# Kernel optimization log

Measured on AMD Instinct MI355X. Metric: run time of the kernel, lower is better.

Reference implementation:

```python
import jax, jax.numpy as jnp
import numpy as np
import math

IN_F = 2048
INTER_F = 8192
OUT_F = 2048
STRIPE = 256
N_STRIPES = INTER_F // STRIPE
EPS = 1e-7
BETA = 0.99
STEPS = 1000.0
THRESH_LR_SCALE = 1.0 * math.sqrt(IN_F)


def setup_inputs() -> dict:
    key = jax.random.key(0)
    ks = jax.random.split(key, 8)
    x = jax.random.normal(ks[0], (2, 1024, IN_F), dtype=jnp.float32)
    gate_weight = jax.random.normal(ks[1], (IN_F, INTER_F), dtype=jnp.float32) / math.sqrt(IN_F)
    gate_bias = jnp.zeros((INTER_F,), dtype=jnp.float32)
    # thresholds ~ threshold_init scale so the mask is non-trivially sparse
    gate_thresholds = jax.random.uniform(ks[2], (N_STRIPES, IN_F), dtype=jnp.float32) * (0.1 / THRESH_LR_SCALE) * 20.0
    med = jax.random.normal(ks[3], (IN_F,), dtype=jnp.float32) * 0.01
    aad = jax.random.uniform(ks[4], (IN_F,), dtype=jnp.float32) + 0.5
    up_weight = jax.random.normal(ks[5], (IN_F, INTER_F), dtype=jnp.float32) * 0.02
    up_bias = jnp.zeros((INTER_F,), dtype=jnp.float32)
    down_weight = jax.random.normal(ks[6], (OUT_F, INTER_F), dtype=jnp.float32) / math.sqrt(INTER_F)
    down_bias = jnp.zeros((OUT_F,), dtype=jnp.float32)
    return dict(x=x, gate_weight=gate_weight, gate_bias=gate_bias,
                gate_thresholds=gate_thresholds, med=med, aad=aad,
                up_weight=up_weight, up_bias=up_bias,
                down_weight=down_weight, down_bias=down_bias)


def _cwic_linear(xf, weight, bias, thresholds, med, aad):
    # eval-mode CWICLinear. xf: [T, I]
    debiaser = 1.0 / (EPS + (1.0 - BETA ** STEPS))
    mu = med * debiaser                                   # [I]
    std = aad * debiaser / math.sqrt(2.0 * math.pi)      # [I]
    thr = thresholds * std[None, :] * THRESH_LR_SCALE     # [N, I]
    xd = xf - mu[None, :]                                 # [T, I]
    mask = (jnp.abs(xd)[:, None, :] > thr[None]).astype(xf.dtype)  # [T, N, I]
    xm = xd[:, None, :] * mask + mu[None, None, :]        # [T, N, I]
    w = weight.T.reshape(N_STRIPES, STRIPE, IN_F)          # [N, S, I]
    y = jnp.einsum('nsi,tni->tns', w, xm).reshape(-1, INTER_F) + bias[None, :]
    active = STRIPE * mask.reshape(xf.shape[0], -1).sum(axis=-1)  # [T]
    dense = jnp.full_like(active, STRIPE * N_STRIPES * IN_F)
    return y, dense, active


def reference(x, gate_weight, gate_bias, gate_thresholds, med, aad,
              up_weight, up_bias, down_weight, down_bias):
    B, T, I = x.shape
    xf = x.reshape(-1, I)
    g, dense, active = _cwic_linear(xf, gate_weight, gate_bias, gate_thresholds, med, aad)
    up = xf @ up_weight + up_bias[None, :]                 # Conv1D: x @ W + b
    h = jax.nn.silu(g) * up                                # [BT, inter]
    y = h @ down_weight.T + down_bias[None, :]             # nn.Linear
    return (y.reshape(B, T, OUT_F), dense.reshape(B, T), active.reshape(B, T))
```

## Files before the change

kernel.cpp:

```cpp
#include <hip/hip_runtime.h>
#include <math.h>
#include <stdint.h>

typedef __bf16 bf16_t;
typedef __bf16 bf16x8 __attribute__((ext_vector_type(8)));
typedef __bf16 bf16x4 __attribute__((ext_vector_type(4)));
typedef float f32x4 __attribute__((ext_vector_type(4)));
typedef short s16x8 __attribute__((ext_vector_type(8)));

#define TOKS 2048
#define INF 2048
#define JNF 8192
#define ONF 2048

#define VMW(N) asm volatile("s_waitcnt vmcnt(" #N ")" ::: "memory")
#define LGKM0 asm volatile("s_waitcnt lgkmcnt(0)" ::: "memory")
#define BAR __builtin_amdgcn_s_barrier()


__device__ __forceinline__ void gld(const bf16_t* g, bf16_t* l) {
  __builtin_amdgcn_global_load_lds((const __attribute__((address_space(1))) void*)g,
                                   (__attribute__((address_space(3))) void*)l, 16, 0, 0);
}
__device__ __forceinline__ void stage2(const bf16_t* p0, const bf16_t* p1, bf16_t* l) {
  gld(p0, l);
  gld(p1, l + 4096);
}

template <int Q>
__device__ __forceinline__ void ds_afq(const bf16_t* A, int a0, int a1, bf16x8 (&af)[2][2]) {
  af[0][0] = *(const bf16x8*)&A[a0 + (Q * 32) * 64];
  af[0][1] = *(const bf16x8*)&A[a1 + (Q * 32) * 64];
  af[1][0] = *(const bf16x8*)&A[a0 + (Q * 32 + 16) * 64];
  af[1][1] = *(const bf16x8*)&A[a1 + (Q * 32 + 16) * 64];
}

__device__ __forceinline__ void ds_bfq(const bf16_t* B, int b0, int b1, bf16x8 (&bfr)[4][2]) {
#pragma unroll
  for (int ni = 0; ni < 4; ++ni) {
    bfr[ni][0] = *(const bf16x8*)&B[b0 + ni * 16 * 64];
    bfr[ni][1] = *(const bf16x8*)&B[b1 + ni * 16 * 64];
  }
}

template <int P>
__device__ __forceinline__ void mfma_ph(f32x4 (&acc)[8][4], const bf16x8 (&af)[2][2],
                                        const bf16x8 (&bfr)[4][2]) {
  constexpr int Q = P & 3;
  __builtin_amdgcn_s_barrier();
  __builtin_amdgcn_s_setprio(1);
#pragma unroll
  for (int mi2 = 0; mi2 < 2; ++mi2)
#pragma unroll
    for (int ni = 0; ni < 4; ++ni)
#pragma unroll
      for (int ks = 0; ks < 2; ++ks)
        acc[Q * 2 + mi2][ni] = __builtin_amdgcn_mfma_f32_16x16x32_bf16(
            af[mi2][ks], bfr[ni][ks], acc[Q * 2 + mi2][ni], 0, 0, 0);
  __builtin_amdgcn_s_setprio(0);
}

__device__ __forceinline__ void mask_tile(bf16_t* At, const bf16_t* Thl,
                                          int ktile, int me0, int kq8) {
  const s16x8 ABS = {0x7FFF, 0x7FFF, 0x7FFF, 0x7FFF, 0x7FFF, 0x7FFF, 0x7FFF, 0x7FFF};
  s16x8 t = *(const s16x8*)&Thl[ktile + kq8];
#pragma unroll
  for (int h = 0; h < 2; ++h)
#pragma unroll
    for (int r = 0; r < 2; ++r) {
      int off = me0 + h * 8192 + r * 4096;
      s16x8 a = *(const s16x8*)&At[off];
      s16x8 m = (s16x8)((t - (a & ABS)) >> 15);
      *(s16x8*)&At[off] = a & m;
    }
}


__global__ __launch_bounds__(256) void prep_mu_thr(
    const float* __restrict__ med, const float* __restrict__ aad,
    const float* __restrict__ gth, float debiaser,
    float* __restrict__ mu, float* __restrict__ thr, bf16_t* __restrict__ thrb) {
  int gid = blockIdx.x * 256 + threadIdx.x;
  if (gid < INF) mu[gid] = med[gid] * debiaser;
  int i = gid & (INF - 1);
  float stdv = aad[i] * debiaser / 2.5066282746310002f;
  float tv = gth[gid] * stdv * 45.254833995939045f;
  thr[gid] = tv;
  thrb[gid] = (bf16_t)tv;
}

__global__ __launch_bounds__(256) void prep_x_count(
    const float* __restrict__ x, const float* __restrict__ mu,
    const float* __restrict__ thr,
    bf16_t* __restrict__ xb, bf16_t* __restrict__ xdb,
    float* __restrict__ dense, float* __restrict__ active) {
  int t = blockIdx.x;
  int tid = threadIdx.x;
  int i0 = tid * 8;
  const float* xrow = x + (size_t)t * INF;
  f32x4 x0 = *(const f32x4*)&xrow[i0];
  f32x4 x1 = *(const f32x4*)&xrow[i0 + 4];
  f32x4 m0 = *(const f32x4*)&mu[i0];
  f32x4 m1 = *(const f32x4*)&mu[i0 + 4];
  f32x4 d0 = x0 - m0, d1 = x1 - m1;
  bf16x8 ox, od;
  ox[0] = (bf16_t)x0[0]; ox[1] = (bf16_t)x0[1]; ox[2] = (bf16_t)x0[2]; ox[3] = (bf16_t)x0[3];
  ox[4] = (bf16_t)x1[0]; ox[5] = (bf16_t)x1[1]; ox[6] = (bf16_t)x1[2]; ox[7] = (bf16_t)x1[3];
  od[0] = (bf16_t)d0[0]; od[1] = (bf16_t)d0[1]; od[2] = (bf16_t)d0[2]; od[3] = (bf16_t)d0[3];
  od[4] = (bf16_t)d1[0]; od[5] = (bf16_t)d1[1]; od[6] = (bf16_t)d1[2]; od[7] = (bf16_t)d1[3];
  *(bf16x8*)&xb[(size_t)t * INF + i0] = ox;
  *(bf16x8*)&xdb[(size_t)t * INF + i0] = od;
  f32x4 a0, a1;
  a0[0] = fabsf(d0[0]); a0[1] = fabsf(d0[1]); a0[2] = fabsf(d0[2]); a0[3] = fabsf(d0[3]);
  a1[0] = fabsf(d1[0]); a1[1] = fabsf(d1[1]); a1[2] = fabsf(d1[2]); a1[3] = fabsf(d1[3]);
  int cnt = 0;
#pragma unroll 4
  for (int n = 0; n < 32; ++n) {
    f32x4 t0 = *(const f32x4*)&thr[(n << 11) + i0];
    f32x4 t1 = *(const f32x4*)&thr[(n << 11) + i0 + 4];
    cnt += (a0[0] > t0[0]) + (a0[1] > t0[1]) + (a0[2] > t0[2]) + (a0[3] > t0[3]);
    cnt += (a1[0] > t1[0]) + (a1[1] > t1[1]) + (a1[2] > t1[2]) + (a1[3] > t1[3]);
  }
  for (int off = 32; off; off >>= 1) cnt += __shfl_down(cnt, off);
  __shared__ int red[4];
  int wv = tid >> 6;
  if ((tid & 63) == 0) red[wv] = cnt;
  __syncthreads();
  if (tid == 0) {
    int tot = red[0] + red[1] + red[2] + red[3];
    active[t] = 256.0f * (float)tot;
    dense[t] = 16777216.0f;
  }
}

__global__ __launch_bounds__(256) void transpose_cast_dual(
    const float* __restrict__ src0, bf16_t* __restrict__ dst0,
    const float* __restrict__ src1, bf16_t* __restrict__ dst1) {
  const float* src = blockIdx.z ? src1 : src0;
  bf16_t* dst = blockIdx.z ? dst1 : dst0;
  __shared__ float tile[64][65];
  int j0 = blockIdx.x * 64;
  int i0 = blockIdx.y * 64;
  int tid = threadIdx.x;
  int r = tid >> 4;
  int c4 = (tid & 15) * 4;
#pragma unroll
  for (int rr = 0; rr < 4; ++rr) {
    int row = rr * 16 + r;
    f32x4 v = *(const f32x4*)&src[(size_t)(i0 + row) * JNF + j0 + c4];
    tile[row][c4] = v[0]; tile[row][c4 + 1] = v[1];
    tile[row][c4 + 2] = v[2]; tile[row][c4 + 3] = v[3];
  }
  __syncthreads();
  int jr = tid >> 3;
  int i8 = (tid & 7) * 8;
#pragma unroll
  for (int rr = 0; rr < 2; ++rr) {
    int jrow = rr * 32 + jr;
    bf16x8 o;
#pragma unroll
    for (int k = 0; k < 8; ++k) o[k] = (bf16_t)tile[i8 + k][jrow];
    *(bf16x8*)&dst[(size_t)(j0 + jrow) * INF + i0 + i8] = o;
  }
}

__global__ __launch_bounds__(256) void cast_bf16(
    const float* __restrict__ src, bf16_t* __restrict__ dst) {
  int idx = (blockIdx.x * 256 + threadIdx.x) * 8;
  f32x4 a = *(const f32x4*)&src[idx];
  f32x4 b = *(const f32x4*)&src[idx + 4];
  bf16x8 o;
  o[0] = (bf16_t)a[0]; o[1] = (bf16_t)a[1]; o[2] = (bf16_t)a[2]; o[3] = (bf16_t)a[3];
  o[4] = (bf16_t)b[0]; o[5] = (bf16_t)b[1]; o[6] = (bf16_t)b[2]; o[7] = (bf16_t)b[3];
  *(bf16x8*)&dst[idx] = o;
}

__global__ __launch_bounds__(256) void c_from_gwT(
    const bf16_t* __restrict__ gwT, const float* __restrict__ mu,
    const float* __restrict__ gb, float* __restrict__ c) {
  int j = blockIdx.x * 4 + (threadIdx.x >> 6);
  int lane = threadIdx.x & 63;
  float s = 0.f;
#pragma unroll
  for (int it = 0; it < 4; ++it) {
    int i = it * 512 + lane * 8;
    bf16x8 w = *(const bf16x8*)&gwT[(size_t)j * INF + i];
    f32x4 m0 = *(const f32x4*)&mu[i];
    f32x4 m1 = *(const f32x4*)&mu[i + 4];
    s += (float)w[0] * m0[0] + (float)w[1] * m0[1] + (float)w[2] * m0[2] + (float)w[3] * m0[3];
    s += (float)w[4] * m1[0] + (float)w[5] * m1[1] + (float)w[6] * m1[2] + (float)w[7] * m1[3];
  }
  for (int off = 32; off; off >>= 1) s += __shfl_down(s, off);
  if (lane == 0) c[j] = gb[j] + s;
}


template <int MODE>
__global__ __launch_bounds__(512) void gemm256(
    const bf16_t* __restrict__ Ag, const bf16_t* __restrict__ Bg,
    const bf16_t* __restrict__ thrv, const float* __restrict__ cvec,
    const bf16_t* __restrict__ gmat, bf16_t* __restrict__ outb,
    float* __restrict__ outf) {
  constexpr size_t LD = (MODE == 1) ? (size_t)JNF : (size_t)INF;
  constexpr int NIT = 16;
  __shared__ bf16_t Als[2][256 * 64];
  __shared__ bf16_t Bls[2][256 * 64];
  __shared__ bf16_t Thl[INF];
  bf16_t* Als0 = Als[0]; bf16_t* Als1 = Als[1];
  bf16_t* Bls0 = Bls[0]; bf16_t* Bls1 = Bls[1];
  int tid = threadIdx.x;
  int lane = tid & 63;
  int wv = tid >> 6;
  int wm = wv >> 2;
  int wn = wv & 3;
  int m16 = lane & 15, q = lane >> 4;
  int t0 = blockIdx.y * 256;
  int j0 = blockIdx.x * 256;
  int kbeg = (MODE == 1) ? blockIdx.z * 2048 : 0;
  const bf16_t* Arow = Ag + (size_t)t0 * LD + kbeg;
  const bf16_t* Brow = Bg + (size_t)j0 * LD + kbeg;

  int rowT = tid >> 3;
  int kq8 = ((tid & 7) ^ (rowT & 7)) * 8;
  const bf16_t* pA0r0 = Arow + (size_t)rowT * LD + kq8;
  const bf16_t* pA0r1 = pA0r0 + (size_t)64 * LD;
  const bf16_t* pA1r0 = pA0r0 + (size_t)128 * LD;
  const bf16_t* pA1r1 = pA0r0 + (size_t)192 * LD;
  const bf16_t* pB0r0 = Brow + (size_t)rowT * LD + kq8;
  const bf16_t* pB0r1 = pB0r0 + (size_t)64 * LD;
  const bf16_t* pB1r0 = pB0r0 + (size_t)128 * LD;
  const bf16_t* pB1r1 = pB0r0 + (size_t)192 * LD;
  int lbase = (tid & ~63) * 8;
  int me0 = rowT * 64 + (tid & 7) * 8;

  int s0 = q ^ (m16 & 7);
  int s1 = (4 + q) ^ (m16 & 7);
  int a0 = (wm * 128 + m16) * 64 + s0 * 8;
  int a1 = (wm * 128 + m16) * 64 + s1 * 8;
  int b0 = (wn * 64 + m16) * 64 + s0 * 8;
  int b1 = (wn * 64 + m16) * 64 + s1 * 8;

  f32x4 acc[8][4] = {};
  bf16x8 bfr[4][2];
  bf16x8 af[2][2];

  if constexpr (MODE == 2) {
    bf16x4 tc = *(const bf16x4*)&thrv[(size_t)blockIdx.x * INF + tid * 4];
    *(bf16x4*)&Thl[tid * 4] = tc;
  }
  stage2(pB0r0, pB0r1, Bls0 + lbase);
  stage2(pB1r0, pB1r1, Bls0 + 8192 + lbase);
  stage2(pA0r0, pA0r1, Als0 + lbase);
  stage2(pA1r0, pA1r1, Als0 + 8192 + lbase);
  stage2(pB0r0 + 64, pB0r1 + 64, Bls1 + lbase);
  stage2(pB1r0 + 64, pB1r1 + 64, Bls1 + 8192 + lbase);
  if constexpr (MODE == 2) {
    VMW(0);
    LGKM0;
    BAR;
    mask_tile(Als0, Thl, 0, me0, kq8);
    LGKM0;
  } else {
    VMW(4);
  }
  BAR;

  for (int i = 0; i < NIT; ++i) {
    const bool S = (i < NIT - 1);
    ds_bfq(Bls0, b0, b1, bfr);
    ds_afq<0>(Als0, a0, a1, af);
    stage2(pA0r0 + 64, pA0r1 + 64, Als1 + lbase);
    mfma_ph<0>(acc, af, bfr); BAR;
    ds_afq<1>(Als0, a0, a1, af);
    stage2(pA1r0 + 64, pA1r1 + 64, Als1 + 8192 + lbase);
    if (S) stage2(pB0r0 + 128, pB0r1 + 128, Bls0 + lbase);
    mfma_ph<1>(acc, af, bfr); BAR;
    ds_afq<2>(Als0, a0, a1, af);
    if (S) stage2(pB1r0 + 128, pB1r1 + 128, Bls0 + 8192 + lbase);
    mfma_ph<2>(acc, af, bfr); BAR;
    ds_afq<3>(Als0, a0, a1, af);
    mfma_ph<3>(acc, af, bfr);
    if (S) { VMW(4); } else { VMW(0); }
    if constexpr (MODE == 2) {
      mask_tile(Als1, Thl, i * 128 + 64, me0, kq8);
      LGKM0;
    }
    BAR;
    ds_bfq(Bls1, b0, b1, bfr);
    ds_afq<0>(Als1, a0, a1, af);
    if (S) stage2(pA0r0 + 128, pA0r1 + 128, Als0 + lbase);
    mfma_ph<4>(acc, af, bfr); BAR;
    ds_afq<1>(Als1, a0, a1, af);
    if (S) stage2(pA1r0 + 128, pA1r1 + 128, Als0 + 8192 + lbase);
    mfma_ph<5>(acc, af, bfr); BAR;
    ds_afq<2>(Als1, a0, a1, af);
    if (S) stage2(pB0r0 + 192, pB0r1 + 192, Bls1 + lbase);
    mfma_ph<6>(acc, af, bfr); BAR;
    ds_afq<3>(Als1, a0, a1, af);
    if (S) stage2(pB1r0 + 192, pB1r1 + 192, Bls1 + 8192 + lbase);
    mfma_ph<7>(acc, af, bfr);
    if (S) { VMW(4); } else { VMW(0); }
    if constexpr (MODE == 2) {
      if (S) {
        mask_tile(Als0, Thl, i * 128 + 128, me0, kq8);
        LGKM0;
      }
    }
    BAR;
    pA0r0 += 128; pA0r1 += 128; pA1r0 += 128; pA1r1 += 128;
    pB0r0 += 128; pB0r1 += 128; pB1r0 += 128; pB1r1 += 128;
  }

  int cb = j0 + wn * 64;
  int rb = t0 + wm * 128;
  if constexpr (MODE == 1) {
    float* dst = outf + (size_t)blockIdx.z * ((size_t)TOKS * ONF);
#pragma unroll
    for (int mi = 0; mi < 8; ++mi)
#pragma unroll
      for (int ni = 0; ni < 4; ++ni) {
        int col = cb + ni * 16 + m16;
#pragma unroll
        for (int r = 0; r < 4; ++r) {
          int row = rb + mi * 16 + q * 4 + r;
          dst[(size_t)row * ONF + col] = acc[mi][ni][r];
        }
      }
  } else if constexpr (MODE == 0) {
#pragma unroll
    for (int mi = 0; mi < 8; ++mi)
#pragma unroll
      for (int ni = 0; ni < 4; ++ni) {
        int col = cb + ni * 16 + m16;
        float bias = cvec[col];
#pragma unroll
        for (int r = 0; r < 4; ++r) {
          int row = rb + mi * 16 + q * 4 + r;
          float upv = acc[mi][ni][r] + bias;
          float gv = (float)gmat[(size_t)row * JNF + col];
          float hv = (gv / (1.f + expf(-gv))) * upv;
          outb[(size_t)row * JNF + col] = (bf16_t)hv;
        }
      }
  } else {
#pragma unroll
    for (int mi = 0; mi < 8; ++mi)
#pragma unroll
      for (int ni = 0; ni < 4; ++ni) {
        int col = cb + ni * 16 + m16;
        float cadd = cvec[col];
#pragma unroll
        for (int r = 0; r < 4; ++r) {
          int row = rb + mi * 16 + q * 4 + r;
          outb[(size_t)row * JNF + col] = (bf16_t)(acc[mi][ni][r] + cadd);
        }
      }
  }
}

__global__ __launch_bounds__(256) void down_reduce(
    const float* __restrict__ part, const float* __restrict__ db,
    float* __restrict__ y) {
  int idx = (blockIdx.x * 256 + threadIdx.x) * 4;
  f32x4 a = *(const f32x4*)&part[idx];
  f32x4 b = *(const f32x4*)&part[idx + 4194304];
  f32x4 c = *(const f32x4*)&part[idx + 2 * 4194304];
  f32x4 d = *(const f32x4*)&part[idx + 3 * 4194304];
  f32x4 bias = *(const f32x4*)&db[idx & (ONF - 1)];
  *(f32x4*)&y[idx] = a + b + c + d + bias;
}


extern "C" void kernel_launch(void* const* d_in, const int* in_sizes, int n_in,
                              void* d_out, int out_size, void* d_ws, size_t ws_size,
                              hipStream_t stream) {
  (void)in_sizes; (void)n_in; (void)out_size; (void)ws_size;
  const float* x   = (const float*)d_in[0];
  const float* gw  = (const float*)d_in[1];
  const float* gb  = (const float*)d_in[2];
  const float* gth = (const float*)d_in[3];
  const float* med = (const float*)d_in[4];
  const float* aad = (const float*)d_in[5];
  const float* uw  = (const float*)d_in[6];
  const float* ub  = (const float*)d_in[7];
  const float* dw  = (const float*)d_in[8];
  const float* db  = (const float*)d_in[9];

  float* out = (float*)d_out;
  float* y = out;
  float* dense = out + 4194304;
  float* active = dense + 2048;

  char* ws = (char*)d_ws;
  float*  mu   = (float*)(ws + 0);
  float*  thr  = (float*)(ws + 8192);
  bf16_t* thrb = (bf16_t*)(ws + 270336);
  float*  cj   = (float*)(ws + 401408);
  bf16_t* xb   = (bf16_t*)(ws + 434176);
  bf16_t* xdb  = (bf16_t*)(ws + 8822784);
  bf16_t* gwT  = (bf16_t*)(ws + 17211392);
  bf16_t* upT  = (bf16_t*)(ws + 50765824);
  bf16_t* dwb  = (bf16_t*)(ws + 84320256);
  bf16_t* hb   = (bf16_t*)(ws + 117874688);
  float*  part = (float*)(ws + 151429120);
  bf16_t* gb16 = (bf16_t*)part;

  float debiaser = (float)(1.0 / (1e-7 + (1.0 - pow(0.99, 1000.0))));

  prep_mu_thr<<<256, 256, 0, stream>>>(med, aad, gth, debiaser, mu, thr, thrb);
  prep_x_count<<<2048, 256, 0, stream>>>(x, mu, thr, xb, xdb, dense, active);
  transpose_cast_dual<<<dim3(128, 32, 2), 256, 0, stream>>>(gw, gwT, uw, upT);
  cast_bf16<<<8192, 256, 0, stream>>>(dw, dwb);
  c_from_gwT<<<2048, 256, 0, stream>>>(gwT, mu, gb, cj);
  gemm256<2><<<dim3(32, 8), 512, 0, stream>>>(xdb, gwT, thrb, cj, nullptr, gb16, nullptr);
  gemm256<0><<<dim3(32, 8), 512, 0, stream>>>(xb, upT, nullptr, ub, gb16, hb, nullptr);
  gemm256<1><<<dim3(8, 8, 4), 512, 0, stream>>>(hb, dwb, nullptr, nullptr, nullptr, nullptr, part);
  down_reduce<<<4096, 256, 0, stream>>>(part, db, y);
}
```

Baseline: 504.9 us.

## Apply threshold mask in registers and store gate in fragment-native layout

Result: slower. 527.8 us (+4.5%).

```diff
diff --git a/kernel.cpp b/kernel.cpp
--- a/kernel.cpp
+++ b/kernel.cpp
@@ -43,11 +43,23 @@
   }
 }
 
-template <int P>
-__device__ __forceinline__ void mfma_ph(f32x4 (&acc)[8][4], const bf16x8 (&af)[2][2],
-                                        const bf16x8 (&bfr)[4][2]) {
-  constexpr int Q = P & 3;
-  __builtin_amdgcn_s_barrier();
+__device__ __forceinline__ bf16x8 maskf(bf16x8 a, bf16x8 t) {
+  const s16x8 ABS = {0x7FFF, 0x7FFF, 0x7FFF, 0x7FFF, 0x7FFF, 0x7FFF, 0x7FFF, 0x7FFF};
+  s16x8 ai = __builtin_bit_cast(s16x8, a);
+  s16x8 ti = __builtin_bit_cast(s16x8, t);
+  s16x8 m = (ti - (ai & ABS)) >> 15;
+  return __builtin_bit_cast(bf16x8, ai & m);
+}
+
+template <int Q, int MODE>
+__device__ __forceinline__ void mfma_q(f32x4 (&acc)[8][4], bf16x8 (&af)[2][2],
+                                       const bf16x8 (&bfr)[4][2], const bf16x8 (&tf)[2]) {
+  if constexpr (MODE == 2) {
+    af[0][0] = maskf(af[0][0], tf[0]);
+    af[0][1] = maskf(af[0][1], tf[1]);
+    af[1][0] = maskf(af[1][0], tf[0]);
+    af[1][1] = maskf(af[1][1], tf[1]);
+  }
   __builtin_amdgcn_s_setprio(1);
 #pragma unroll
   for (int mi2 = 0; mi2 < 2; ++mi2)
@@ -58,21 +70,6 @@
         acc[Q * 2 + mi2][ni] = __builtin_amdgcn_mfma_f32_16x16x32_bf16(
             af[mi2][ks], bfr[ni][ks], acc[Q * 2 + mi2][ni], 0, 0, 0);
   __builtin_amdgcn_s_setprio(0);
-}
-
-__device__ __forceinline__ void mask_tile(bf16_t* At, const bf16_t* Thl,
-                                          int ktile, int me0, int kq8) {
-  const s16x8 ABS = {0x7FFF, 0x7FFF, 0x7FFF, 0x7FFF, 0x7FFF, 0x7FFF, 0x7FFF, 0x7FFF};
-  s16x8 t = *(const s16x8*)&Thl[ktile + kq8];
-#pragma unroll
-  for (int h = 0; h < 2; ++h)
-#pragma unroll
-    for (int r = 0; r < 2; ++r) {
-      int off = me0 + h * 8192 + r * 4096;
-      s16x8 a = *(const s16x8*)&At[off];
-      s16x8 m = (s16x8)((t - (a & ABS)) >> 15);
-      *(s16x8*)&At[off] = a & m;
-    }
 }
 
 
@@ -231,7 +228,6 @@
   const bf16_t* pB1r0 = pB0r0 + (size_t)128 * LD;
   const bf16_t* pB1r1 = pB0r0 + (size_t)192 * LD;
   int lbase = (tid & ~63) * 8;
-  int me0 = rowT * 64 + (tid & 7) * 8;
 
   int s0 = q ^ (m16 & 7);
   int s1 = (4 + q) ^ (m16 & 7);
@@ -243,6 +239,7 @@
   f32x4 acc[8][4] = {};
   bf16x8 bfr[4][2];
   bf16x8 af[2][2];
+  bf16x8 tf[2] = {};
 
   if constexpr (MODE == 2) {
     bf16x4 tc = *(const bf16x4*)&thrv[(size_t)blockIdx.x * INF + tid * 4];
@@ -254,58 +251,57 @@
   stage2(pA1r0, pA1r1, Als0 + 8192 + lbase);
   stage2(pB0r0 + 64, pB0r1 + 64, Bls1 + lbase);
   stage2(pB1r0 + 64, pB1r1 + 64, Bls1 + 8192 + lbase);
-  if constexpr (MODE == 2) {
-    VMW(0);
-    LGKM0;
-    BAR;
-    mask_tile(Als0, Thl, 0, me0, kq8);
-    LGKM0;
-  } else {
-    VMW(4);
-  }
+  VMW(4);
+  if constexpr (MODE == 2) { LGKM0; }
   BAR;
 
   for (int i = 0; i < NIT; ++i) {
     const bool S = (i < NIT - 1);
     ds_bfq(Bls0, b0, b1, bfr);
     ds_afq<0>(Als0, a0, a1, af);
+    if constexpr (MODE == 2) {
+      tf[0] = *(const bf16x8*)&Thl[i * 128 + q * 8];
+      tf[1] = *(const bf16x8*)&Thl[i * 128 + 32 + q * 8];
+    }
+    BAR;
     stage2(pA0r0 + 64, pA0r1 + 64, Als1 + lbase);
-    mfma_ph<0>(acc, af, bfr); BAR;
+    mfma_q<0, MODE>(acc, af, bfr, tf);
     ds_afq<1>(Als0, a0, a1, af);
+    BAR;
     stage2(pA1r0 + 64, pA1r1 + 64, Als1 + 8192 + lbase);
+    mfma_q<1, MODE>(acc, af, bfr, tf);
+    ds_afq<2>(Als0, a0, a1, af);
+    BAR;
     if (S) stage2(pB0r0 + 128, pB0r1 + 128, Bls0 + lbase);
-    mfma_ph<1>(acc, af, bfr); BAR;
-    ds_afq<2>(Als0, a0, a1, af);
+    mfma_q<2, MODE>(acc, af, bfr, tf);
+    ds_afq<3>(Als0, a0, a1, af);
+    BAR;
     if (S) stage2(pB1r0 + 128, pB1r1 + 128, Bls0 + 8192 + lbase);
-    mfma_ph<2>(acc, af, bfr); BAR;
-    ds_afq<3>(Als0, a0, a1, af);
-    mfma_ph<3>(acc, af, bfr);
+    mfma_q<3, MODE>(acc, af, bfr, tf);
     if (S) { VMW(4); } else { VMW(0); }
-    if constexpr (MODE == 2) {
-      mask_tile(Als1, Thl, i * 128 + 64, me0, kq8);
-      LGKM0;
-    }
     BAR;
     ds_bfq(Bls1, b0, b1, bfr);
     ds_afq<0>(Als1, a0, a1, af);
+    if constexpr (MODE == 2) {
+      tf[0] = *(const bf16x8*)&Thl[i * 128 + 64 + q * 8];
+      tf[1] = *(const bf16x8*)&Thl[i * 128 + 96 + q * 8];
+    }
+    BAR;
     if (S) stage2(pA0r0 + 128, pA0r1 + 128, Als0 + lbase);
-    mfma_ph<4>(acc, af, bfr); BAR;
+    mfma_q<0, MODE>(acc, af, bfr, tf);
     ds_afq<1>(Als1, a0, a1, af);
+    BAR;
     if (S) stage2(pA1r0 + 128, pA1r1 + 128, Als0 + 8192 + lbase);
-    mfma_ph<5>(acc, af, bfr); BAR;
+    mfma_q<1, MODE>(acc, af, bfr, tf);
     ds_afq<2>(Als1, a0, a1, af);
+    BAR;
     if (S) stage2(pB0r0 + 192, pB0r1 + 192, Bls1 + lbase);
-    mfma_ph<6>(acc, af, bfr); BAR;
+    mfma_q<2, MODE>(acc, af, bfr, tf);
     ds_afq<3>(Als1, a0, a1, af);
+    BAR;
     if (S) stage2(pB1r0 + 192, pB1r1 + 192, Bls1 + 8192 + lbase);
-    mfma_ph<7>(acc, af, bfr);
+    mfma_q<3, MODE>(acc, af, bfr, tf);
     if (S) { VMW(4); } else { VMW(0); }
-    if constexpr (MODE == 2) {
-      if (S) {
-        mask_tile(Als0, Thl, i * 128 + 128, me0, kq8);
-        LGKM0;
-      }
-    }
     BAR;
     pA0r0 += 128; pA0r1 += 128; pA1r0 += 128; pA1r1 += 128;
     pB0r0 += 128; pB0r1 += 128; pB1r0 += 128; pB1r1 += 128;
@@ -327,6 +323,10 @@
         }
       }
   } else if constexpr (MODE == 0) {
+    size_t gbse = ((size_t)(blockIdx.x * 8 + blockIdx.y)) * 65536 + (size_t)tid * 8;
+    bf16x8 gvv[16];
+#pragma unroll
+    for (int v = 0; v < 16; ++v) gvv[v] = *(const bf16x8*)&gmat[gbse + (size_t)v * 4096];
 #pragma unroll
     for (int mi = 0; mi < 8; ++mi)
 #pragma unroll
@@ -337,24 +337,28 @@
         for (int r = 0; r < 4; ++r) {
           int row = rb + mi * 16 + q * 4 + r;
           float upv = acc[mi][ni][r] + bias;
-          float gv = (float)gmat[(size_t)row * JNF + col];
+          float gv = (float)gvv[mi * 2 + (ni >> 1)][(ni & 1) * 4 + r];
           float hv = (gv / (1.f + expf(-gv))) * upv;
           outb[(size_t)row * JNF + col] = (bf16_t)hv;
         }
       }
   } else {
-#pragma unroll
-    for (int mi = 0; mi < 8; ++mi)
-#pragma unroll
-      for (int ni = 0; ni < 4; ++ni) {
-        int col = cb + ni * 16 + m16;
-        float cadd = cvec[col];
-#pragma unroll
-        for (int r = 0; r < 4; ++r) {
-          int row = rb + mi * 16 + q * 4 + r;
-          outb[(size_t)row * JNF + col] = (bf16_t)(acc[mi][ni][r] + cadd);
-        }
+    size_t gbse = ((size_t)(blockIdx.x * 8 + blockIdx.y)) * 65536 + (size_t)tid * 8;
+    float ca[4];
+#pragma unroll
+    for (int ni = 0; ni < 4; ++ni) ca[ni] = cvec[cb + ni * 16 + m16];
+#pragma unroll
+    for (int v = 0; v < 16; ++v) {
+      int mi = v >> 1;
+      bf16x8 o;
+#pragma unroll
+      for (int e = 0; e < 8; ++e) {
+        int ni = (v & 1) * 2 + (e >> 2);
+        int r = e & 3;
+        o[e] = (bf16_t)(acc[mi][ni][r] + ca[ni]);
       }
+      *(bf16x8*)&outb[gbse + (size_t)v * 4096] = o;
+    }
   }
 }
 
```
